# Kernel tuning notes

Measured on AMD Instinct MI355X. Metric: run time of the kernel, lower is better.

Reference implementation:

```python
import jax, jax.numpy as jnp
import numpy as np

B, S, D = 1, 2048, 2048
H, KV, HD = 32, 8, 64  # heads, kv heads, head_dim
THETA = 10000.0


def rot(x):
    # torch: cat(-x[..., d/2:], x[..., :d/2])
    f, s = jnp.split(x, 2, axis=-1)
    return jnp.concatenate((-s, f), axis=-1)


def setup_inputs() -> dict:
    key = jax.random.key(0)
    k0, k1, k2, k3, k4 = jax.random.split(key, 5)
    x = jax.random.normal(k0, (B, S, D), jnp.float32)
    Wq = jax.random.normal(k1, (H * HD, D), jnp.float32) * 0.02
    Wk = jax.random.normal(k2, (KV * HD, D), jnp.float32) * 0.02
    Wv = jax.random.normal(k3, (KV * HD, D), jnp.float32) * 0.02
    Wo = jax.random.normal(k4, (D, H * HD), jnp.float32) * 0.02
    inv_freq = 1.0 / (THETA ** (jnp.arange(0, HD, 2, dtype=jnp.float32) / HD))
    return {"x": x, "Wq": Wq, "Wk": Wk, "Wv": Wv, "Wo": Wo, "inv_freq": inv_freq}


def reference(x, Wq, Wk, Wv, Wo, inv_freq):
    bsz, seqlen, _ = x.shape
    q = (x @ Wq.T).reshape(bsz, seqlen, H, HD).transpose(0, 2, 1, 3)   # [B,H,S,hd]
    k = (x @ Wk.T).reshape(bsz, seqlen, KV, HD).transpose(0, 2, 1, 3)  # [B,KV,S,hd]
    v = (x @ Wv.T).reshape(bsz, seqlen, KV, HD).transpose(0, 2, 1, 3)

    # RoPE cos/sin (computed under no_grad in torch)
    pos = jnp.arange(seqlen, dtype=jnp.float32)
    freqs = pos[:, None] * inv_freq[None, :]                # [S, hd/2]
    emb = jnp.concatenate((freqs, freqs), axis=-1)          # [S, hd]
    cos = jnp.cos(emb)[None, None]                          # [1,1,S,hd]
    sin = jnp.sin(emb)[None, None]
    q = q * cos + rot(q) * sin
    k = k * cos + rot(k) * sin

    # GQA: group query heads per kv head instead of repeat_interleaving kv
    G = H // KV
    qg = q.reshape(bsz, KV, G, seqlen, HD)
    scores = jnp.einsum('bkgsd,bktd->bkgst', qg, k) / jnp.sqrt(jnp.float32(HD))
    mask = jnp.triu(jnp.full((seqlen, seqlen), -jnp.inf, jnp.float32), 1)
    attn = jax.nn.softmax(scores + mask, axis=-1)
    out = jnp.einsum('bkgst,bktd->bkgsd', attn, v)          # [B,KV,G,S,hd]
    out = out.reshape(bsz, H, seqlen, HD).transpose(0, 2, 1, 3).reshape(bsz, seqlen, H * HD)
    return out @ Wo.T
```

## Files before the change

kernel.cpp:

```cpp
#include <hip/hip_runtime.h>
#include <hip/hip_bf16.h>
#include <math.h>

#define S_LEN 2048
#define D_MODEL 2048
#define N_H 32
#define N_KV 8
#define HD 64

typedef __attribute__((ext_vector_type(8))) short short8;
typedef __attribute__((ext_vector_type(4))) float floatx4;
typedef unsigned short u16;
typedef unsigned int u32;

#define QSCALE 0.18033688011112042f

#if defined(__has_builtin)
#if __has_builtin(__builtin_amdgcn_exp2f)
#define EXP2(x) __builtin_amdgcn_exp2f(x)
#else
#define EXP2(x) __expf(0.6931471805599453f * (x))
#endif
#else
#define EXP2(x) __expf(0.6931471805599453f * (x))
#endif

__device__ __forceinline__ u16 f2bf(float f) {
    union { float f; u32 u; } v; v.f = f;
    u32 r = v.u + 0x7fffu + ((v.u >> 16) & 1u);
    return (u16)(r >> 16);
}
__device__ __forceinline__ u16 f2bf_fast(float f) {
    union { float f; u32 u; } v; v.f = f;
    return (u16)((v.u + 0x8000u) >> 16);
}

__device__ __forceinline__ void gload16(const void* gp, void* lp) {
    __builtin_amdgcn_global_load_lds(
        (const __attribute__((address_space(1))) unsigned int*)gp,
        (__attribute__((address_space(3))) unsigned int*)lp,
        16, 0, 0);
}

__global__ __launch_bounds__(256) void cast_all(const float* __restrict__ x,
                                                const float* __restrict__ Wq,
                                                const float* __restrict__ Wk,
                                                const float* __restrict__ Wv,
                                                const float* __restrict__ Wo,
                                                u16* __restrict__ xb,
                                                u16* __restrict__ wqkv,
                                                u16* __restrict__ wob) {
    const int i = (blockIdx.x * 256 + threadIdx.x) * 4;
    const int row = i >> 11;
    const int col = i & 2047;
    const float* src;
    u16* dst;
    if (row < 2048)      { src = x  + (size_t)row * 2048 + col;          dst = xb + i; }
    else if (row < 4096) { src = Wq + (size_t)(row - 2048) * 2048 + col; dst = wqkv + (i - 2048 * 2048); }
    else if (row < 4608) { src = Wk + (size_t)(row - 4096) * 2048 + col; dst = wqkv + (i - 2048 * 2048); }
    else if (row < 5120) { src = Wv + (size_t)(row - 4608) * 2048 + col; dst = wqkv + (i - 2048 * 2048); }
    else                 { src = Wo + (size_t)(row - 5120) * 2048 + col; dst = wob + (i - 5120 * 2048); }
    const float4 v = *(const float4*)src;
    ushort4 o;
    o.x = f2bf(v.x); o.y = f2bf(v.y); o.z = f2bf(v.z); o.w = f2bf(v.w);
    *(ushort4*)dst = o;
}

__global__ __launch_bounds__(256) void gemm_qkv(const u16* __restrict__ A,
                                                const u16* __restrict__ B,
                                                u16* __restrict__ Qh,
                                                u16* __restrict__ Kh,
                                                u16* __restrict__ Vt,
                                                const float* __restrict__ inv_freq,
                                                int K) {
    __shared__ u16 As[2][64 * 32];
    __shared__ u16 Bs[2][128 * 32];
    const int tid  = threadIdx.x;
    const int w    = tid >> 6;
    const int lane = tid & 63;
    const int lr   = lane & 15;
    const int quad = lane >> 4;
    const int bm = blockIdx.x * 64, bn = blockIdx.y * 128;
    const int wm = (w & 1) * 32, wn = (w >> 1) * 64;

    const int srow = tid >> 2;
    const int sch  = (tid & 3) * 8;
    const u16* Ag = A + (size_t)(bm + srow) * K + sch;
    const u16* Bg = B + (size_t)(bn + srow) * K + sch;
    const int loff = srow * 32 + sch;
    const size_t gstride = (size_t)64 * K;

    floatx4 acc[2][4];
#pragma unroll
    for (int i = 0; i < 2; ++i)
#pragma unroll
        for (int j = 0; j < 4; ++j) acc[i][j] = floatx4{0.f, 0.f, 0.f, 0.f};

    gload16(Ag, &As[0][loff]);
    gload16(Bg, &Bs[0][loff]);
    gload16(Bg + gstride, &Bs[0][loff + 64 * 32]);
    __syncthreads();

    for (int k0 = 0; k0 < K; k0 += 32) {
        const int cur = (k0 >> 5) & 1;
        if (k0 + 32 < K) {
            gload16(Ag + k0 + 32, &As[cur ^ 1][loff]);
            gload16(Bg + k0 + 32, &Bs[cur ^ 1][loff]);
            gload16(Bg + gstride + k0 + 32, &Bs[cur ^ 1][loff + 64 * 32]);
        }
        short8 af[2], bf[4];
#pragma unroll
        for (int t = 0; t < 2; ++t)
            af[t] = *(const short8*)&As[cur][(wm + t * 16 + lr) * 32 + quad * 8];
#pragma unroll
        for (int t = 0; t < 4; ++t)
            bf[t] = *(const short8*)&Bs[cur][(wn + t * 16 + lr) * 32 + quad * 8];
#pragma unroll
        for (int im = 0; im < 2; ++im)
#pragma unroll
            for (int in = 0; in < 4; ++in)
                acc[im][in] = __builtin_amdgcn_mfma_f32_16x16x32_bf16(
                    af[im], bf[in], acc[im][in], 0, 0, 0);
        __syncthreads();
    }

    const int c0 = bn + wn;
    if (bn < 2048) {
        const int h = c0 >> 6;
#pragma unroll
        for (int p = 0; p < 2; ++p) {
            const int d = p * 16 + lr;
            const float fr = inv_freq[d];
#pragma unroll
            for (int im = 0; im < 2; ++im)
#pragma unroll
                for (int r = 0; r < 4; ++r) {
                    const int s = bm + wm + im * 16 + quad * 4 + r;
                    float sn, cs;
                    sincosf((float)s * fr, &sn, &cs);
                    const float xl = acc[im][p][r], xh = acc[im][p + 2][r];
                    u16* qrow = Qh + ((size_t)h * S_LEN + s) * HD;
                    qrow[d]      = f2bf((xl * cs - xh * sn) * QSCALE);
                    qrow[d + 32] = f2bf((xh * cs + xl * sn) * QSCALE);
                }
        }
    } else if (bn < 2560) {
        const int kv = (c0 - 2048) >> 6;
#pragma unroll
        for (int p = 0; p < 2; ++p) {
            const int d = p * 16 + lr;
            const float fr = inv_freq[d];
#pragma unroll
            for (int im = 0; im < 2; ++im)
#pragma unroll
                for (int r = 0; r < 4; ++r) {
                    const int s = bm + wm + im * 16 + quad * 4 + r;
                    float sn, cs;
                    sincosf((float)s * fr, &sn, &cs);
                    const float xl = acc[im][p][r], xh = acc[im][p + 2][r];
                    u16* krow = Kh + ((size_t)kv * S_LEN + s) * HD;
                    krow[d]      = f2bf(xl * cs - xh * sn);
                    krow[d + 32] = f2bf(xh * cs + xl * sn);
                }
        }
    } else {
        const int kv = (c0 - 2560) >> 6;
#pragma unroll
        for (int im = 0; im < 2; ++im)
#pragma unroll
            for (int in = 0; in < 4; ++in) {
                const int dfull = in * 16 + lr;
                const int s0 = bm + wm + im * 16 + quad * 4;
                ushort4 o;
                o.x = f2bf(acc[im][in][0]); o.y = f2bf(acc[im][in][1]);
                o.z = f2bf(acc[im][in][2]); o.w = f2bf(acc[im][in][3]);
                *(ushort4*)&Vt[((size_t)kv * HD + dfull) * S_LEN + s0] = o;
            }
    }
}

__global__ __launch_bounds__(256) void gemm_out(const u16* __restrict__ A,
                                                const u16* __restrict__ B,
                                                float* __restrict__ Cf,
                                                int N, int K) {
    __shared__ u16 As[2][64 * 32];
    __shared__ u16 Bs[2][64 * 32];
    const int tid  = threadIdx.x;
    const int w    = tid >> 6;
    const int lane = tid & 63;
    const int lr   = lane & 15;
    const int quad = lane >> 4;
    const int bm = blockIdx.x * 64, bn = blockIdx.y * 64;
    const int wm = w * 16;

    const int srow = tid >> 2;
    const int sch  = (tid & 3) * 8;
    const u16* Ag = A + (size_t)(bm + srow) * K + sch;
    const u16* Bg = B + (size_t)(bn + srow) * K + sch;
    const int loff = srow * 32 + sch;

    floatx4 acc[4];
#pragma unroll
    for (int j = 0; j < 4; ++j) acc[j] = floatx4{0.f, 0.f, 0.f, 0.f};

    gload16(Ag, &As[0][loff]);
    gload16(Bg, &Bs[0][loff]);
    __syncthreads();

    for (int k0 = 0; k0 < K; k0 += 32) {
        const int cur = (k0 >> 5) & 1;
        if (k0 + 32 < K) {
            gload16(Ag + k0 + 32, &As[cur ^ 1][loff]);
            gload16(Bg + k0 + 32, &Bs[cur ^ 1][loff]);
        }
        short8 af, bf[4];
        af = *(const short8*)&As[cur][(wm + lr) * 32 + quad * 8];
#pragma unroll
        for (int in = 0; in < 4; ++in)
            bf[in] = *(const short8*)&Bs[cur][(in * 16 + lr) * 32 + quad * 8];
#pragma unroll
        for (int in = 0; in < 4; ++in)
            acc[in] = __builtin_amdgcn_mfma_f32_16x16x32_bf16(
                af, bf[in], acc[in], 0, 0, 0);
        __syncthreads();
    }

#pragma unroll
    for (int in = 0; in < 4; ++in) {
        const int row0 = bm + wm + quad * 4;
        const int col  = bn + in * 16 + lr;
#pragma unroll
        for (int r = 0; r < 4; ++r)
            Cf[(size_t)(row0 + r) * N + col] = acc[in][r];
    }
}

__global__ __launch_bounds__(256) void attn_mfma(const u16* __restrict__ Qh,
                                                 const u16* __restrict__ Kh,
                                                 const u16* __restrict__ Vt,
                                                 u16* __restrict__ AO) {
    __shared__ u16 QPs[64 * 64];
    __shared__ u16 Ks[2][64 * 64];
    __shared__ u16 Vs[2][64 * 64];

    const int bid = blockIdx.x;
    const int h   = bid & 31;
    const int qb  = 31 - (bid >> 5);
    const int kv  = h >> 2;
    const int tid  = threadIdx.x;
    const int w    = tid >> 6;
    const int lr   = tid & 15;
    const int quad = (tid >> 4) & 3;
    const int grow = tid >> 3;
    const int gp   = tid & 7;

    const u16* Qg = Qh + ((size_t)h * S_LEN + (size_t)qb * 64) * HD;
    const u16* Kg = Kh + (size_t)kv * S_LEN * HD;
    const u16* Vg = Vt + (size_t)kv * HD * S_LEN;

#pragma unroll
    for (int j = 0; j < 2; ++j) {
        const int r = j * 32 + grow;
        gload16(Qg + (size_t)r * HD + ((gp ^ (r & 7)) * 8), QPs + r * 64 + gp * 8);
        gload16(Kg + (size_t)r * HD + ((gp ^ (r & 7)) * 8), &Ks[0][r * 64 + gp * 8]);
        gload16(Vg + (size_t)r * S_LEN + ((gp ^ (r & 7)) * 8), &Vs[0][r * 64 + gp * 8]);
    }
    __syncthreads();

    const int wq0 = qb * 64 + w * 16;

    short8 qf[2];
#pragma unroll
    for (int kh = 0; kh < 2; ++kh) {
        const int row = w * 16 + lr;
        const int c   = kh * 4 + quad;
        qf[kh] = *(const short8*)&QPs[row * 64 + ((c ^ (row & 7)) * 8)];
    }

    float l_st[4] = {0.f, 0.f, 0.f, 0.f};
    floatx4 oacc[4];
#pragma unroll
    for (int dn = 0; dn < 4; ++dn) oacc[dn] = floatx4{0.f, 0.f, 0.f, 0.f};

    for (int kt = 0; kt <= qb; ++kt) {
        const int buf = kt & 1;
        if (kt < qb) {
            const int nb = buf ^ 1;
#pragma unroll
            for (int j = 0; j < 2; ++j) {
                const int r = j * 32 + grow;
                gload16(Kg + (size_t)((kt + 1) * 64 + r) * HD + ((gp ^ (r & 7)) * 8),
                        &Ks[nb][r * 64 + gp * 8]);
                gload16(Vg + (size_t)r * S_LEN + (kt + 1) * 64 + ((gp ^ (r & 7)) * 8),
                        &Vs[nb][r * 64 + gp * 8]);
            }
        }
        if (64 * kt <= wq0 + 15) {
            floatx4 st[4];
#pragma unroll
            for (int in = 0; in < 4; ++in) st[in] = floatx4{0.f, 0.f, 0.f, 0.f};
#pragma unroll
            for (int in = 0; in < 4; ++in)
#pragma unroll
                for (int kh = 0; kh < 2; ++kh) {
                    const int row = in * 16 + lr;
                    const int c   = kh * 4 + quad;
                    const short8 kf = *(const short8*)
                        &Ks[buf][row * 64 + ((c ^ (row & 7)) * 8)];
                    st[in] = __builtin_amdgcn_mfma_f32_16x16x32_bf16(
                        qf[kh], kf, st[in], 0, 0, 0);
                }

            const bool need_mask = (kt * 64 + 63) > wq0;
#pragma unroll
            for (int r = 0; r < 4; ++r) {
                float ps = 0.f;
#pragma unroll
                for (int in = 0; in < 4; ++in) {
                    float s = st[in][r];
                    if (need_mask) {
                        const int rg = wq0 + quad * 4 + r;
                        const int cg = kt * 64 + in * 16 + lr;
                        if (cg > rg) s = -1e30f;
                    }
                    const float p = EXP2(s);
                    st[in][r] = p;
                    ps += p;
                }
                l_st[r] += ps;
            }

#pragma unroll
            for (int in = 0; in < 4; ++in)
#pragma unroll
                for (int r = 0; r < 4; ++r) {
                    const int prow = w * 16 + quad * 4 + r;
                    const int col  = in * 16 + lr;
                    QPs[prow * 64 + (((col >> 3) ^ (prow & 7)) * 8) + (col & 7)] =
                        f2bf_fast(st[in][r]);
                }

#pragma unroll
            for (int kc = 0; kc < 2; ++kc) {
                const int prow = w * 16 + lr;
                const short8 pf = *(const short8*)
                    &QPs[prow * 64 + (((kc * 4 + quad) ^ (prow & 7)) * 8)];
#pragma unroll
                for (int dn = 0; dn < 4; ++dn) {
                    const int vrow = dn * 16 + lr;
                    const int c    = kc * 4 + quad;
                    const short8 vf = *(const short8*)
                        &Vs[buf][vrow * 64 + ((c ^ (vrow & 7)) * 8)];
                    oacc[dn] = __builtin_amdgcn_mfma_f32_16x16x32_bf16(
                        pf, vf, oacc[dn], 0, 0, 0);
                }
            }
        }
        __syncthreads();
    }

#pragma unroll
    for (int r = 0; r < 4; ++r) {
        float lv = l_st[r];
#pragma unroll
        for (int mk = 1; mk < 16; mk <<= 1)
            lv += __shfl_xor(lv, mk);
        const float inv = 1.f / lv;
        const size_t row = (size_t)(wq0 + quad * 4 + r);
#pragma unroll
        for (int dn = 0; dn < 4; ++dn)
            AO[row * D_MODEL + h * 64 + dn * 16 + lr] =
                f2bf(oacc[dn][r] * inv);
    }
}

extern "C" void kernel_launch(void* const* d_in, const int* in_sizes, int n_in,
                              void* d_out, int out_size, void* d_ws, size_t ws_size,
                              hipStream_t stream) {
    const float* x        = (const float*)d_in[0];
    const float* Wq       = (const float*)d_in[1];
    const float* Wk       = (const float*)d_in[2];
    const float* Wv       = (const float*)d_in[3];
    const float* Wo       = (const float*)d_in[4];
    const float* inv_freq = (const float*)d_in[5];
    float* out = (float*)d_out;

    const size_t ME = 1 << 20;
    u16* xb   = (u16*)d_ws;
    u16* wqkv = xb   + 4 * ME;
    u16* wob  = wqkv + 6 * ME;
    u16* qhb  = wob  + 4 * ME;
    u16* khb  = qhb  + 4 * ME;
    u16* vtb  = khb  + 1 * ME;
    u16* aob  = vtb  + 1 * ME;

    const dim3 b256(256);

    cast_all<<<14336, b256, 0, stream>>>(x, Wq, Wk, Wv, Wo, xb, wqkv, wob);

    gemm_qkv<<<dim3(32, 24), b256, 0, stream>>>(
        xb, wqkv, qhb, khb, vtb, inv_freq, D_MODEL);

    attn_mfma<<<dim3(1024), b256, 0, stream>>>(qhb, khb, vtb, aob);

    gemm_out<<<dim3(32, 32), b256, 0, stream>>>(
        aob, wob, out, D_MODEL, D_MODEL);
}
```

Before: 222.4 us.

## Swizzle QKV GEMM block order and deepen out-proj K tile with XOR LDS layout

The QKV projection kernel remaps the linear block id so that consecutive blocks spread across N tiles, aiming for better L2 reuse of the A and B panels. The output projection GEMM doubles its K step from 32 to 64 per iteration. It stores tiles in LDS with an XOR-swizzled column layout to avoid bank conflicts on the wider rows, and halves the number of barriers per K. This doubles the shared memory used by gemm_out, which may reduce occupancy. The swizzle also hard-codes the grid shape (32 x 24 blocks).

```diff
diff --git a/kernel.cpp b/kernel.cpp
--- a/kernel.cpp
+++ b/kernel.cpp
@@ -80,7 +80,11 @@
     const int lane = tid & 63;
     const int lr   = lane & 15;
     const int quad = lane >> 4;
-    const int bm = blockIdx.x * 64, bn = blockIdx.y * 128;
+
+    const int bid = blockIdx.y * 32 + blockIdx.x;
+    const int swz = (bid & 7) * 96 + (bid >> 3);
+    const int bm = (swz & 31) * 64;
+    const int bn = (swz >> 5) * 128;
     const int wm = (w & 1) * 32, wn = (w >> 1) * 64;
 
     const int srow = tid >> 2;
@@ -183,8 +187,8 @@
                                                 const u16* __restrict__ B,
                                                 float* __restrict__ Cf,
                                                 int N, int K) {
-    __shared__ u16 As[2][64 * 32];
-    __shared__ u16 Bs[2][64 * 32];
+    __shared__ u16 As[2][64 * 64];
+    __shared__ u16 Bs[2][64 * 64];
     const int tid  = threadIdx.x;
     const int w    = tid >> 6;
     const int lane = tid & 63;
@@ -193,35 +197,55 @@
     const int bm = blockIdx.x * 64, bn = blockIdx.y * 64;
     const int wm = w * 16;
 
-    const int srow = tid >> 2;
-    const int sch  = (tid & 3) * 8;
-    const u16* Ag = A + (size_t)(bm + srow) * K + sch;
-    const u16* Bg = B + (size_t)(bn + srow) * K + sch;
-    const int loff = srow * 32 + sch;
+    const int srow = tid >> 3;
+    const int sch  = tid & 7;
 
     floatx4 acc[4];
 #pragma unroll
     for (int j = 0; j < 4; ++j) acc[j] = floatx4{0.f, 0.f, 0.f, 0.f};
 
-    gload16(Ag, &As[0][loff]);
-    gload16(Bg, &Bs[0][loff]);
+#pragma unroll
+    for (int j = 0; j < 2; ++j) {
+        const int r = j * 32 + srow;
+        gload16(A + (size_t)(bm + r) * K + ((sch ^ (r & 7)) * 8),
+                &As[0][r * 64 + sch * 8]);
+        gload16(B + (size_t)(bn + r) * K + ((sch ^ (r & 7)) * 8),
+                &Bs[0][r * 64 + sch * 8]);
+    }
     __syncthreads();
 
-    for (int k0 = 0; k0 < K; k0 += 32) {
-        const int cur = (k0 >> 5) & 1;
-        if (k0 + 32 < K) {
-            gload16(Ag + k0 + 32, &As[cur ^ 1][loff]);
-            gload16(Bg + k0 + 32, &Bs[cur ^ 1][loff]);
-        }
-        short8 af, bf[4];
-        af = *(const short8*)&As[cur][(wm + lr) * 32 + quad * 8];
-#pragma unroll
-        for (int in = 0; in < 4; ++in)
-            bf[in] = *(const short8*)&Bs[cur][(in * 16 + lr) * 32 + quad * 8];
-#pragma unroll
-        for (int in = 0; in < 4; ++in)
-            acc[in] = __builtin_amdgcn_mfma_f32_16x16x32_bf16(
-                af, bf[in], acc[in], 0, 0, 0);
+    for (int k0 = 0; k0 < K; k0 += 64) {
+        const int cur = (k0 >> 6) & 1;
+        if (k0 + 64 < K) {
+            const int nb = cur ^ 1;
+#pragma unroll
+            for (int j = 0; j < 2; ++j) {
+                const int r = j * 32 + srow;
+                gload16(A + (size_t)(bm + r) * K + k0 + 64 + ((sch ^ (r & 7)) * 8),
+                        &As[nb][r * 64 + sch * 8]);
+                gload16(B + (size_t)(bn + r) * K + k0 + 64 + ((sch ^ (r & 7)) * 8),
+                        &Bs[nb][r * 64 + sch * 8]);
+            }
+        }
+#pragma unroll
+        for (int kk = 0; kk < 2; ++kk) {
+            short8 af, bf[4];
+            {
+                const int row = wm + lr;
+                const int c   = kk * 4 + quad;
+                af = *(const short8*)&As[cur][row * 64 + ((c ^ (row & 7)) * 8)];
+            }
+#pragma unroll
+            for (int in = 0; in < 4; ++in) {
+                const int row = in * 16 + lr;
+                const int c   = kk * 4 + quad;
+                bf[in] = *(const short8*)&Bs[cur][row * 64 + ((c ^ (row & 7)) * 8)];
+            }
+#pragma unroll
+            for (int in = 0; in < 4; ++in)
+                acc[in] = __builtin_amdgcn_mfma_f32_16x16x32_bf16(
+                    af, bf[in], acc[in], 0, 0, 0);
+        }
         __syncthreads();
     }
 
```

Result: faster. 212.8 us (-4.3%).
